# Performance work log

Measured on AMD Instinct MI355X. Metric: run time of the kernel, lower is better.

Reference implementation:

```python
import jax, jax.numpy as jnp
import numpy as np

WS = (2, 7, 7)      # window size
SS = (1, 3, 3)      # shift size
NH = 8              # num heads
DIM = 256
N = WS[0] * WS[1] * WS[2]   # 98 tokens per window
EPS = 1e-5


def _ln(x, w, b):
    m = jnp.mean(x, -1, keepdims=True)
    v = jnp.mean((x - m) ** 2, -1, keepdims=True)
    return (x - m) / jnp.sqrt(v + EPS) * w + b


def _rel_index():
    coords = np.stack(np.meshgrid(np.arange(WS[0]), np.arange(WS[1]), np.arange(WS[2]), indexing='ij'))
    cf = coords.reshape(3, -1)
    rc = (cf[:, :, None] - cf[:, None, :]).transpose(1, 2, 0).astype(np.int64)
    rc[..., 0] += WS[0] - 1
    rc[..., 1] += WS[1] - 1
    rc[..., 2] += WS[2] - 1
    rc[..., 0] *= (2 * WS[1] - 1) * (2 * WS[2] - 1)
    rc[..., 1] *= 2 * WS[2] - 1
    return rc.sum(-1).astype(np.int32)  # [N, N]


def _attn_mask(Dp, Hp, Wp):
    img = np.zeros((1, Dp, Hp, Wp, 1), np.float32)
    cnt = 0
    def sl(ws, ss):
        return (slice(0, -ws), slice(-ws, -ss), slice(-ss, None))
    for d in sl(WS[0], SS[0]):
        for h in sl(WS[1], SS[1]):
            for w in sl(WS[2], SS[2]):
                img[:, d, h, w, :] = cnt
                cnt += 1
    mw = img.reshape(1, Dp // WS[0], WS[0], Hp // WS[1], WS[1], Wp // WS[2], WS[2], 1)
    mw = mw.transpose(0, 1, 3, 5, 2, 4, 6, 7).reshape(-1, N)
    am = mw[:, None, :] - mw[:, :, None]
    return np.where(am != 0, np.float32(-100.0), np.float32(0.0)).astype(np.float32)  # [nW, N, N]


def setup_inputs() -> dict:
    key = jax.random.key(0)
    ks = jax.random.split(key, 6)
    B, D, H, W, C = 2, 16, 56, 56, DIM
    hid = 4 * C
    return {
        'x': jax.random.normal(ks[0], (B, D, H, W, C), jnp.float32),
        'mask_matrix': jnp.asarray(_attn_mask(D, H, W)),
        'rel_index': jnp.asarray(_rel_index()),
        'rel_bias_table': 0.02 * jax.random.normal(ks[1], ((2 * WS[0] - 1) * (2 * WS[1] - 1) * (2 * WS[2] - 1), NH), jnp.float32),
        'norm1_w': jnp.ones((C,), jnp.float32), 'norm1_b': jnp.zeros((C,), jnp.float32),
        'qkv_w': 0.02 * jax.random.normal(ks[2], (3 * C, C), jnp.float32), 'qkv_b': jnp.zeros((3 * C,), jnp.float32),
        'proj_w': 0.02 * jax.random.normal(ks[3], (C, C), jnp.float32), 'proj_b': jnp.zeros((C,), jnp.float32),
        'norm2_w': jnp.ones((C,), jnp.float32), 'norm2_b': jnp.zeros((C,), jnp.float32),
        'fc1_w': 0.02 * jax.random.normal(ks[4], (hid, C), jnp.float32), 'fc1_b': jnp.zeros((hid,), jnp.float32),
        'fc2_w': 0.02 * jax.random.normal(ks[5], (C, hid), jnp.float32), 'fc2_b': jnp.zeros((C,), jnp.float32),
    }


def _forward(x, mask_matrix, rel_index, rel_bias_table, norm1_w, norm1_b, qkv_w, qkv_b,
             proj_w, proj_b, norm2_w, norm2_b, fc1_w, fc1_b, fc2_w, fc2_b):
    B, D, H, W, C = x.shape
    nh, hd = NH, C // NH
    scale = hd ** -0.5
    nd, nhw, nww = D // WS[0], H // WS[1], W // WS[2]

    # --- part 1: norm -> shift -> window attention -> unshift ---
    h = _ln(x, norm1_w, norm1_b)
    h = jnp.roll(h, (-SS[0], -SS[1], -SS[2]), axis=(1, 2, 3))
    # window partition -> [B_, N, C]
    h = h.reshape(B, nd, WS[0], nhw, WS[1], nww, WS[2], C)
    h = h.transpose(0, 1, 3, 5, 2, 4, 6, 7).reshape(-1, N, C)
    B_ = h.shape[0]

    qkv = (h @ qkv_w.T + qkv_b).reshape(B_, N, 3, nh, hd).transpose(2, 0, 3, 1, 4)
    q, k, v = qkv[0], qkv[1], qkv[2]   # [B_, nh, N, hd]
    attn = jnp.einsum('bhnd,bhmd->bhnm', q * scale, k)
    bias = rel_bias_table[rel_index.reshape(-1)].reshape(N, N, nh).transpose(2, 0, 1)
    attn = attn + bias[None]
    nW = mask_matrix.shape[0]
    attn = attn.reshape(B_ // nW, nW, nh, N, N) + mask_matrix[None, :, None]
    attn = jax.nn.softmax(attn.reshape(B_, nh, N, N), axis=-1)
    o = jnp.einsum('bhnm,bhmd->bhnd', attn, v).transpose(0, 2, 1, 3).reshape(B_, N, C)
    o = o @ proj_w.T + proj_b
    # window reverse -> [B, D, H, W, C]
    o = o.reshape(B, nd, nhw, nww, WS[0], WS[1], WS[2], C)
    o = o.transpose(0, 1, 4, 2, 5, 3, 6, 7).reshape(B, D, H, W, C)
    o = jnp.roll(o, SS, axis=(1, 2, 3))

    x = x + o
    # --- part 2: MLP ---
    h2 = _ln(x, norm2_w, norm2_b)
    h2 = jax.nn.gelu(h2 @ fc1_w.T + fc1_b, approximate=False)
    return x + (h2 @ fc2_w.T + fc2_b)


def reference(x, mask_matrix, rel_index, rel_bias_table, norm1_w, norm1_b, qkv_w, qkv_b,
              proj_w, proj_b, norm2_w, norm2_b, fc1_w, fc1_b, fc2_w, fc2_b):
    return _forward(x, mask_matrix, rel_index, rel_bias_table, norm1_w, norm1_b, qkv_w, qkv_b,
                    proj_w, proj_b, norm2_w, norm2_b, fc1_w, fc1_b, fc2_w, fc2_b)
```

## Files before the change

kernel.cpp:

```cpp
#include <hip/hip_runtime.h>
#include <hip/hip_bf16.h>

typedef __attribute__((ext_vector_type(8))) short bf16x8;
typedef __attribute__((ext_vector_type(4))) float f32x4;

__device__ __forceinline__ unsigned short f2bf(float f){
  __hip_bfloat16 h = __float2bfloat16(f);
  return *reinterpret_cast<unsigned short*>(&h);
}

#define GLDS16(gptr, lptr) \
  __builtin_amdgcn_global_load_lds((const __attribute__((address_space(1))) unsigned int*)(gptr), \
                                   (__attribute__((address_space(3))) unsigned int*)(lptr), 16, 0, 0)

__global__ void cvtk(const float* __restrict__ s, unsigned short* __restrict__ d, int n){
  int i = blockIdx.x*256 + threadIdx.x;
  if (i < n) d[i] = f2bf(s[i]);
}

__global__ void combok(const int* __restrict__ ri, const float* __restrict__ tbl,
                       const float* __restrict__ mask, unsigned short* __restrict__ out){
  int g = blockIdx.x*256 + threadIdx.x;
  if (g >= 802816) return;
  int r = g & 3;
  int t = g >> 2;
  int lane = t & 63; t >>= 6;
  int nt = t % 7; t /= 7;
  int mt = t % 7; t /= 7;
  int p = t >> 3, h = t & 7;
  int gi = mt*16 + (lane >> 4)*4 + r; if (gi > 97) gi = 97;
  int j  = nt*16 + (lane & 15);
  float v;
  if (j < 98){
    int wrep = ((p&4)?448:0) + ((p&2)?56:0) + ((p&1)?7:0);
    v = tbl[ri[gi*98 + j]*8 + h] + mask[(size_t)wrep*9604 + gi*98 + j];
  } else {
    v = -30000.f;
  }
  out[g] = f2bf(v);
}

__launch_bounds__(256)
__global__ void lnk(const float* __restrict__ xin, const float* __restrict__ gw, const float* __restrict__ gb,
                    unsigned short* __restrict__ hout, int mode)
{
  int wid = threadIdx.x >> 6, lane = threadIdx.x & 63;
  int tok = blockIdx.x*4 + wid;
  int src;
  if (mode == 0){
    int w = tok / 98, n = tok % 98;
    int b = w >> 9, rr = w & 511;
    int di = rr >> 6, hi = (rr >> 3) & 7, wi = rr & 7;
    int d2 = n / 49, n2 = n % 49, h2 = n2 / 7, w2 = n2 % 7;
    int sd = (di*2 + d2 + 1) & 15;
    int sh = hi*7 + h2 + 3; if (sh >= 56) sh -= 56;
    int sw = wi*7 + w2 + 3; if (sw >= 56) sw -= 56;
    src = ((b*16 + sd)*56 + sh)*56 + sw;
  } else {
    src = tok;
  }
  float4 v = *(const float4*)(xin + (size_t)src*256 + lane*4);
  float s  = v.x + v.y + v.z + v.w;
  float s2 = v.x*v.x + v.y*v.y + v.z*v.z + v.w*v.w;
  #pragma unroll
  for (int off = 1; off < 64; off <<= 1){
    s  += __shfl_xor(s, off);
    s2 += __shfl_xor(s2, off);
  }
  float mean = s * (1.f/256.f);
  float var  = s2 * (1.f/256.f) - mean*mean;
  float rstd = rsqrtf(var + 1e-5f);
  int c = lane*4;
  float4 wv = *(const float4*)(gw + c);
  float4 bv = *(const float4*)(gb + c);
  unsigned int p0 = (unsigned int)f2bf((v.x-mean)*rstd*wv.x + bv.x)
                  | ((unsigned int)f2bf((v.y-mean)*rstd*wv.y + bv.y) << 16);
  unsigned int p1 = (unsigned int)f2bf((v.z-mean)*rstd*wv.z + bv.z)
                  | ((unsigned int)f2bf((v.w-mean)*rstd*wv.w + bv.w) << 16);
  uint2 pk; pk.x = p0; pk.y = p1;
  *(uint2*)(hout + (size_t)tok*256 + c) = pk;
}

template<int EPI>
__launch_bounds__(256, 4)
__global__ void gemmk(const unsigned short* __restrict__ A, const unsigned short* __restrict__ Bw,
                      const float* __restrict__ bias, int K, int nbx,
                      unsigned short* __restrict__ outb, const float* __restrict__ xres,
                      float* __restrict__ outf, int moff)
{
  __shared__ unsigned short As[2][4096];
  __shared__ unsigned short Bs[2][4096];
  int tid = threadIdx.x;
  int wid = tid >> 6, lane = tid & 63, l16 = lane & 15, lk = lane >> 4;
  int wm = wid >> 1, wn = wid & 1;
  int cpx = gridDim.x >> 3;
  int swb = (blockIdx.x & 7)*cpx + (blockIdx.x >> 3);
  int mblk = swb / nbx, nblk = swb % nbx;
  const unsigned short* Ab = A  + (size_t)mblk*128*K;
  const unsigned short* Bb = Bw + (size_t)nblk*128*K;
  int rA = tid >> 2;
  int kcA = (((tid & 3) ^ ((tid >> 3) & 3)))*8;
  int sx = (l16 >> 1) & 3;

#define STAGE(bufi, kss) do { \
    GLDS16(Ab + (size_t)rA*K      + (kss) + kcA, &As[bufi][wid*512]); \
    GLDS16(Ab + (size_t)(rA+64)*K + (kss) + kcA, &As[bufi][2048 + wid*512]); \
    GLDS16(Bb + (size_t)rA*K      + (kss) + kcA, &Bs[bufi][wid*512]); \
    GLDS16(Bb + (size_t)(rA+64)*K + (kss) + kcA, &Bs[bufi][2048 + wid*512]); \
  } while(0)

  f32x4 acc[4][4];
  #pragma unroll
  for (int i = 0; i < 4; i++)
    #pragma unroll
    for (int j = 0; j < 4; j++)
      acc[i][j] = (f32x4){0.f,0.f,0.f,0.f};

  STAGE(0, 0);
  __syncthreads();
  int cur = 0;
  for (int ks = 0; ks < K; ks += 32){
    if (ks + 32 < K) STAGE(cur ^ 1, ks + 32);
    bf16x8 af[4], bfr[4];
    #pragma unroll
    for (int mi = 0; mi < 4; mi++) af[mi]  = *(const bf16x8*)&As[cur][(wm*64 + mi*16 + l16)*32 + (lk ^ sx)*8];
    #pragma unroll
    for (int ni = 0; ni < 4; ni++) bfr[ni] = *(const bf16x8*)&Bs[cur][(wn*64 + ni*16 + l16)*32 + (lk ^ sx)*8];
    #pragma unroll
    for (int mi = 0; mi < 4; mi++)
      #pragma unroll
      for (int ni = 0; ni < 4; ni++)
        acc[mi][ni] = __builtin_amdgcn_mfma_f32_16x16x32_bf16(af[mi], bfr[ni], acc[mi][ni], 0, 0, 0);
    __syncthreads();
    cur ^= 1;
  }
#undef STAGE

  int rowb = mblk*128 + wm*64;
  int colb = nblk*128 + wn*64;
  #pragma unroll
  for (int mi = 0; mi < 4; mi++){
    #pragma unroll
    for (int r = 0; r < 4; r++){
      int row = rowb + mi*16 + lk*4 + r;
      if constexpr (EPI == 0){
        #pragma unroll
        for (int ni = 0; ni < 4; ni++){
          int col = colb + ni*16 + l16;
          float v = acc[mi][ni][r] + bias[col];
          if (col < 256) v *= 0.17677669529663687f;
          outb[(size_t)row*768 + col] = f2bf(v);
        }
      } else if constexpr (EPI == 1){
        int w = row / 98, n = row % 98;
        int b = w >> 9, rr = w & 511;
        int di = rr >> 6, hi = (rr >> 3) & 7, wi = rr & 7;
        int d2 = n / 49, n2 = n % 49, h2 = n2 / 7, w2 = n2 % 7;
        int sd = (di*2 + d2 + 1) & 15;
        int sh = hi*7 + h2 + 3; if (sh >= 56) sh -= 56;
        int sw = wi*7 + w2 + 3; if (sw >= 56) sw -= 56;
        size_t tnat = (((size_t)b*16 + sd)*56 + sh)*56 + sw;
        #pragma unroll
        for (int ni = 0; ni < 4; ni++){
          int col = colb + ni*16 + l16;
          float v = acc[mi][ni][r] + bias[col];
          outf[tnat*256 + col] = xres[tnat*256 + col] + v;
        }
      } else if constexpr (EPI == 2){
        #pragma unroll
        for (int ni = 0; ni < 4; ni++){
          int col = colb + ni*16 + l16;
          float v = acc[mi][ni][r] + bias[col];
          float gl = v * 0.5f * (1.f + erff(v * 0.70710678118654752f));
          outb[(size_t)row*1024 + col] = f2bf(gl);
        }
      } else {
        #pragma unroll
        for (int ni = 0; ni < 4; ni++){
          int col = colb + ni*16 + l16;
          float v = acc[mi][ni][r] + bias[col];
          outf[((size_t)(moff + row))*256 + col] += v;
        }
      }
    }
  }
}

__launch_bounds__(256)
__global__ void attnk(const unsigned short* __restrict__ qkv, const unsigned short* __restrict__ comboX,
                      unsigned short* __restrict__ obuf)
{
  __shared__ unsigned short P[4][16*136];
  int tid = threadIdx.x, wid = tid >> 6, lane = tid & 63, l16 = lane & 15, lk = lane >> 4;
  int cpx = gridDim.x >> 3;
  int swb = (blockIdx.x & 7)*cpx + (blockIdx.x >> 3);
  int task = swb*4 + wid;
  int w = task >> 3, h = task & 7;
  int rr = w & 511;
  int pat = (((rr>>6)==7)?4:0) | ((((rr>>3)&7)==7)?2:0) | (((rr&7)==7)?1:0);
  const unsigned short* cb = comboX + (size_t)(pat*8 + h)*12544;
  const unsigned short* base = qkv + (size_t)w*98*768 + h*32;

  bf16x8 kfr[7];
  #pragma unroll
  for (int nt = 0; nt < 7; nt++){
    int kc = nt*16 + l16; if (kc > 97) kc = 97;
    kfr[nt] = *(const bf16x8*)(base + (size_t)kc*768 + 256 + lk*8);
  }
  bf16x8 v0[4], v1[4];
  #pragma unroll
  for (int kcc = 0; kcc < 4; kcc++){
    #pragma unroll
    for (int j = 0; j < 8; j++){
      int k = kcc*32 + lk*8 + j; if (k > 97) k = 97;
      unsigned int u = *(const unsigned int*)(base + (size_t)k*768 + 512 + 2*l16);
      v0[kcc][j] = (short)(u & 0xffff);
      v1[kcc][j] = (short)(u >> 16);
    }
  }
  bf16x8 vones;
  #pragma unroll
  for (int j = 0; j < 8; j++) vones[j] = (short)0x3F80;

  unsigned short* Pw = &P[wid][0];
  { int rp = lane >> 2, cc = 112 + (lane & 3)*4;
    *(uint2*)&Pw[rp*136 + cc] = make_uint2(0u, 0u); }

  for (int mt = 0; mt < 7; mt++){
    int qrow = mt*16 + l16; if (qrow > 97) qrow = 97;
    bf16x8 qa = *(const bf16x8*)(base + (size_t)qrow*768 + lk*8);

    const unsigned short* cm = cb + mt*1792;
    f32x4 s[7];
    #pragma unroll
    for (int nt = 0; nt < 7; nt++){
      uint2 c2 = *(const uint2*)(cm + (nt*64 + lane)*4);
      f32x4 ci;
      ci[0] = __uint_as_float(c2.x << 16);
      ci[1] = __uint_as_float(c2.x & 0xffff0000u);
      ci[2] = __uint_as_float(c2.y << 16);
      ci[3] = __uint_as_float(c2.y & 0xffff0000u);
      s[nt] = __builtin_amdgcn_mfma_f32_16x16x32_bf16(qa, kfr[nt], ci, 0, 0, 0);
    }

    float mx[4] = {-3e38f,-3e38f,-3e38f,-3e38f};
    #pragma unroll
    for (int nt = 0; nt < 7; nt++){
      mx[0] = fmaxf(mx[0], s[nt][0]); mx[1] = fmaxf(mx[1], s[nt][1]);
      mx[2] = fmaxf(mx[2], s[nt][2]); mx[3] = fmaxf(mx[3], s[nt][3]);
    }
    float mxa = fmaxf(fmaxf(mx[0], mx[1]), fmaxf(mx[2], mx[3]));
    #pragma unroll
    for (int off = 1; off < 64; off <<= 1) mxa = fmaxf(mxa, __shfl_xor(mxa, off));

    #pragma unroll
    for (int r = 0; r < 4; r++)
      #pragma unroll
      for (int nt = 0; nt < 7; nt++)
        Pw[(lk*4 + r)*136 + nt*16 + l16] = f2bf(__expf(s[nt][r] - mxa));

    f32x4 o0 = (f32x4){0.f,0.f,0.f,0.f}, o1 = (f32x4){0.f,0.f,0.f,0.f};
    f32x4 os = (f32x4){0.f,0.f,0.f,0.f};
    #pragma unroll
    for (int kcc = 0; kcc < 4; kcc++){
      bf16x8 pa = *(const bf16x8*)&Pw[l16*136 + kcc*32 + lk*8];
      __builtin_amdgcn_s_setprio(1);
      o0 = __builtin_amdgcn_mfma_f32_16x16x32_bf16(pa, v0[kcc], o0, 0, 0, 0);
      o1 = __builtin_amdgcn_mfma_f32_16x16x32_bf16(pa, v1[kcc], o1, 0, 0, 0);
      os = __builtin_amdgcn_mfma_f32_16x16x32_bf16(pa, vones,   os, 0, 0, 0);
      __builtin_amdgcn_s_setprio(0);
    }
    #pragma unroll
    for (int r = 0; r < 4; r++){
      int n = mt*16 + lk*4 + r;
      if (n < 98){
        float inv = __builtin_amdgcn_rcpf(os[r]);
        unsigned int pk = (unsigned int)f2bf(o0[r]*inv) | ((unsigned int)f2bf(o1[r]*inv) << 16);
        *(unsigned int*)(obuf + ((size_t)w*98 + n)*256 + h*32 + 2*l16) = pk;
      }
    }
  }
}

extern "C" void kernel_launch(void* const* d_in, const int* in_sizes, int n_in,
                              void* d_out, int out_size, void* d_ws, size_t ws_size,
                              hipStream_t stream)
{
  const float* x     = (const float*)d_in[0];
  const float* maskm = (const float*)d_in[1];
  const int*   ri    = (const int*)d_in[2];
  const float* tbl   = (const float*)d_in[3];
  const float* n1w   = (const float*)d_in[4];
  const float* n1b   = (const float*)d_in[5];
  const float* qkvw  = (const float*)d_in[6];
  const float* qkvbv = (const float*)d_in[7];
  const float* projw = (const float*)d_in[8];
  const float* projb = (const float*)d_in[9];
  const float* n2w   = (const float*)d_in[10];
  const float* n2b   = (const float*)d_in[11];
  const float* fc1w  = (const float*)d_in[12];
  const float* fc1b  = (const float*)d_in[13];
  const float* fc2w  = (const float*)d_in[14];
  const float* fc2b  = (const float*)d_in[15];
  float* dout = (float*)d_out;
  char* ws = (char*)d_ws;

  unsigned short* qkvB  = (unsigned short*)(ws + 0);
  unsigned short* hb    = (unsigned short*)(ws + 154140672);
  unsigned short* wq    = (unsigned short*)(ws + 205520896);
  unsigned short* comboX= (unsigned short*)(ws + 205914112);
  unsigned short* wp    = (unsigned short*)(ws + 0);
  unsigned short* h2 = (unsigned short*)(ws + 0);
  unsigned short* g  = (unsigned short*)(ws + 51380224);
  unsigned short* w1 = (unsigned short*)(ws + 154140672);
  unsigned short* w2 = (unsigned short*)(ws + 154664960);

  cvtk<<<768, 256, 0, stream>>>(qkvw, wq, 196608);
  combok<<<3136, 256, 0, stream>>>(ri, tbl, maskm, comboX);

  lnk<<<25088, 256, 0, stream>>>(x, n1w, n1b, hb, 0);
  gemmk<0><<<784*6, 256, 0, stream>>>(hb, wq, qkvbv, 256, 6, qkvB, nullptr, nullptr, 0);
  attnk<<<2048, 256, 0, stream>>>(qkvB, comboX, hb);
  cvtk<<<256, 256, 0, stream>>>(projw, wp, 65536);
  gemmk<1><<<784*2, 256, 0, stream>>>(hb, wp, projb, 256, 2, nullptr, x, dout, 0);

  cvtk<<<1024, 256, 0, stream>>>(fc1w, w1, 262144);
  cvtk<<<1024, 256, 0, stream>>>(fc2w, w2, 262144);
  lnk<<<25088, 256, 0, stream>>>(dout, n2w, n2b, h2, 1);
  for (int c = 0; c < 2; c++){
    gemmk<2><<<392*8, 256, 0, stream>>>(h2 + (size_t)c*50176*256, w1, fc1b, 256, 8, g, nullptr, nullptr, 0);
    gemmk<3><<<392*2, 256, 0, stream>>>(g, w2, fc2b, 1024, 2, nullptr, nullptr, dout, c*50176);
  }
}
```

Measured before the change: 485.7 us.

## Permute GEMM B-tile rows so epilogue writes contiguous 4-column vectors

```diff
diff --git a/kernel.cpp b/kernel.cpp
--- a/kernel.cpp
+++ b/kernel.cpp
@@ -16,6 +16,13 @@
 __global__ void cvtk(const float* __restrict__ s, unsigned short* __restrict__ d, int n){
   int i = blockIdx.x*256 + threadIdx.x;
   if (i < n) d[i] = f2bf(s[i]);
+}
+
+__global__ void cvt2k(const float* __restrict__ s1, int n1, const float* __restrict__ s2, int n2,
+                      unsigned short* __restrict__ d){
+  int i = blockIdx.x*256 + threadIdx.x;
+  if (i < n1) d[i] = f2bf(s1[i]);
+  else if (i < n1 + n2) d[i] = f2bf(s2[i - n1]);
 }
 
 __global__ void combok(const int* __restrict__ ri, const float* __restrict__ tbl,
@@ -99,14 +106,15 @@
   const unsigned short* Ab = A  + (size_t)mblk*128*K;
   const unsigned short* Bb = Bw + (size_t)nblk*128*K;
   int rA = tid >> 2;
+  int rB = ((rA & 15) << 2) + ((rA >> 4) & 3);
   int kcA = (((tid & 3) ^ ((tid >> 3) & 3)))*8;
   int sx = (l16 >> 1) & 3;
 
 #define STAGE(bufi, kss) do { \
     GLDS16(Ab + (size_t)rA*K      + (kss) + kcA, &As[bufi][wid*512]); \
     GLDS16(Ab + (size_t)(rA+64)*K + (kss) + kcA, &As[bufi][2048 + wid*512]); \
-    GLDS16(Bb + (size_t)rA*K      + (kss) + kcA, &Bs[bufi][wid*512]); \
-    GLDS16(Bb + (size_t)(rA+64)*K + (kss) + kcA, &Bs[bufi][2048 + wid*512]); \
+    GLDS16(Bb + (size_t)rB*K      + (kss) + kcA, &Bs[bufi][wid*512]); \
+    GLDS16(Bb + (size_t)(rB+64)*K + (kss) + kcA, &Bs[bufi][2048 + wid*512]); \
   } while(0)
 
   f32x4 acc[4][4];
@@ -138,19 +146,26 @@
 
   int rowb = mblk*128 + wm*64;
   int colb = nblk*128 + wn*64;
+  int c4 = colb + 4*l16;
+  float4 bv = *(const float4*)(bias + c4);
   #pragma unroll
   for (int mi = 0; mi < 4; mi++){
     #pragma unroll
     for (int r = 0; r < 4; r++){
       int row = rowb + mi*16 + lk*4 + r;
+      float v0 = acc[mi][0][r] + bv.x;
+      float v1 = acc[mi][1][r] + bv.y;
+      float v2 = acc[mi][2][r] + bv.z;
+      float v3 = acc[mi][3][r] + bv.w;
       if constexpr (EPI == 0){
-        #pragma unroll
-        for (int ni = 0; ni < 4; ni++){
-          int col = colb + ni*16 + l16;
-          float v = acc[mi][ni][r] + bias[col];
-          if (col < 256) v *= 0.17677669529663687f;
-          outb[(size_t)row*768 + col] = f2bf(v);
+        if (colb < 256){
+          const float sc = 0.17677669529663687f;
+          v0 *= sc; v1 *= sc; v2 *= sc; v3 *= sc;
         }
+        uint2 pk;
+        pk.x = (unsigned int)f2bf(v0) | ((unsigned int)f2bf(v1) << 16);
+        pk.y = (unsigned int)f2bf(v2) | ((unsigned int)f2bf(v3) << 16);
+        *(uint2*)(outb + (size_t)row*768 + c4) = pk;
       } else if constexpr (EPI == 1){
         int w = row / 98, n = row % 98;
         int b = w >> 9, rr = w & 511;
@@ -160,27 +175,24 @@
         int sh = hi*7 + h2 + 3; if (sh >= 56) sh -= 56;
         int sw = wi*7 + w2 + 3; if (sw >= 56) sw -= 56;
         size_t tnat = (((size_t)b*16 + sd)*56 + sh)*56 + sw;
-        #pragma unroll
-        for (int ni = 0; ni < 4; ni++){
-          int col = colb + ni*16 + l16;
-          float v = acc[mi][ni][r] + bias[col];
-          outf[tnat*256 + col] = xres[tnat*256 + col] + v;
-        }
+        float4 xr = *(const float4*)(xres + tnat*256 + c4);
+        float4 ov;
+        ov.x = xr.x + v0; ov.y = xr.y + v1; ov.z = xr.z + v2; ov.w = xr.w + v3;
+        *(float4*)(outf + tnat*256 + c4) = ov;
       } else if constexpr (EPI == 2){
-        #pragma unroll
-        for (int ni = 0; ni < 4; ni++){
-          int col = colb + ni*16 + l16;
-          float v = acc[mi][ni][r] + bias[col];
-          float gl = v * 0.5f * (1.f + erff(v * 0.70710678118654752f));
-          outb[(size_t)row*1024 + col] = f2bf(gl);
-        }
+        float g0 = v0 * 0.5f * (1.f + erff(v0 * 0.70710678118654752f));
+        float g1 = v1 * 0.5f * (1.f + erff(v1 * 0.70710678118654752f));
+        float g2 = v2 * 0.5f * (1.f + erff(v2 * 0.70710678118654752f));
+        float g3 = v3 * 0.5f * (1.f + erff(v3 * 0.70710678118654752f));
+        uint2 pk;
+        pk.x = (unsigned int)f2bf(g0) | ((unsigned int)f2bf(g1) << 16);
+        pk.y = (unsigned int)f2bf(g2) | ((unsigned int)f2bf(g3) << 16);
+        *(uint2*)(outb + (size_t)row*1024 + c4) = pk;
       } else {
-        #pragma unroll
-        for (int ni = 0; ni < 4; ni++){
-          int col = colb + ni*16 + l16;
-          float v = acc[mi][ni][r] + bias[col];
-          outf[((size_t)(moff + row))*256 + col] += v;
-        }
+        float* p = outf + (size_t)(moff + row)*256 + c4;
+        float4 cu = *(const float4*)p;
+        cu.x += v0; cu.y += v1; cu.z += v2; cu.w += v3;
+        *(float4*)p = cu;
       }
     }
   }
@@ -324,8 +336,7 @@
   cvtk<<<256, 256, 0, stream>>>(projw, wp, 65536);
   gemmk<1><<<784*2, 256, 0, stream>>>(hb, wp, projb, 256, 2, nullptr, x, dout, 0);
 
-  cvtk<<<1024, 256, 0, stream>>>(fc1w, w1, 262144);
-  cvtk<<<1024, 256, 0, stream>>>(fc2w, w2, 262144);
+  cvt2k<<<2048, 256, 0, stream>>>(fc1w, 262144, fc2w, 262144, w1);
   lnk<<<25088, 256, 0, stream>>>(dout, n2w, n2b, h2, 1);
   for (int c = 0; c < 2; c++){
     gemmk<2><<<392*8, 256, 0, stream>>>(h2 + (size_t)c*50176*256, w1, fc1b, 256, 8, g, nullptr, nullptr, 0);
```

Result: faster. 458.3 us (-5.6%).
